# Optimization experiments

Hardware: AMD Instinct MI355X
Metric: run time of the kernel (lower is better)

The kernel has to match this reference:

```python
import jax, jax.numpy as jnp
import numpy as np

HOPS = 3  # max_hops; C has HOPS+1 tables

def setup_inputs() -> dict:
    key = jax.random.key(0)
    k1, k2, k3 = jax.random.split(key, 3)
    B, M, S, V, D = 32, 512, 10, 32000, 128
    story = jax.random.randint(k1, (B, M, S), 0, V)
    hidden = jax.random.normal(k2, (B, 1, D), dtype=jnp.float32)
    # hop+1 embedding tables, initialized N(0, 0.1) like the torch module
    C = 0.1 * jax.random.normal(k3, (HOPS + 1, V, D), dtype=jnp.float32)
    return {"story": story, "hidden": hidden, "C": C}

def reference(story, hidden, C):
    # story: [B, M, S] int tokens; hidden: [B, 1, D]; C: [HOPS+1, V, D]
    u = jnp.squeeze(hidden, axis=1)  # [B, D]
    prob_logit = None
    for h in range(HOPS):
        # embedding gather + bag-sum over sentence dim -> [B, M, D]
        embed_A = jnp.take(C[h], story, axis=0).sum(axis=2)
        # dot-product attention logits against current query u
        prob_logit = jnp.einsum('bmd,bd->bm', embed_A, u)  # [B, M]
        prob = jax.nn.softmax(prob_logit, axis=1)
        # second table gather + bag-sum, then softmax-weighted combine
        embed_C = jnp.take(C[h + 1], story, axis=0).sum(axis=2)  # [B, M, D]
        o_k = jnp.einsum('bm,bmd->bd', prob, embed_C)  # [B, D]
        u = u + o_k
    return prob_logit, u
```

## Files before the change

kernel.cpp:

```cpp
#include <hip/hip_runtime.h>

#define BB 32
#define MM 512
#define SS 10
#define VV 32000
#define DD 128
#define HOPS 3
#define BM (BB * MM)
#define NCHUNK 32
#define CHM (MM / NCHUNK)
#define PSTRIDE 132


__device__ __forceinline__ void write_partial(const int b, const int c,
                                              const int w, const int lane,
                                              float nx, float ny, float den,
                                              float* __restrict__ pout,
                                              float (*sx)[64], float (*sy)[64],
                                              float* sd) {
    sx[w][lane] = nx; sy[w][lane] = ny;
    if (lane == 0) sd[w] = den;
    __syncthreads();
    if (w == 0) {
        const float ox = sx[0][lane] + sx[1][lane] + sx[2][lane] + sx[3][lane];
        const float oy = sy[0][lane] + sy[1][lane] + sy[2][lane] + sy[3][lane];
        float* prow = pout + ((size_t)b * NCHUNK + c) * PSTRIDE;
        ((float2*)prow)[lane] = make_float2(ox, oy);
        if (lane == 0) prow[DD] = sd[0] + sd[1] + sd[2] + sd[3];
    }
}

__global__ __launch_bounds__(256) void hop0_k(const int* __restrict__ story,
                                              const float* __restrict__ C0,
                                              const float* __restrict__ C1,
                                              const float* __restrict__ hidden,
                                              float* __restrict__ E1,
                                              float* __restrict__ P0) {
    const int b = blockIdx.y, c = blockIdx.x;
    const int tid = threadIdx.x;
    const int w = tid >> 6, lane = tid & 63;
    __shared__ float su[DD];
    __shared__ float sx[4][64], sy[4][64];
    __shared__ float sd[4];

    if (tid < DD) su[tid] = hidden[b * DD + tid];
    __syncthreads();
    const float2 uv = ((const float2*)su)[lane];

    float nx = 0.f, ny = 0.f, den = 0.f;
#pragma unroll
    for (int k = 0; k < CHM / 4; ++k) {
        const int m = c * CHM + k * 4 + w;
        const int bm = b * MM + m;
        int tok[SS];
        const int* st = story + (size_t)bm * SS;
#pragma unroll
        for (int s = 0; s < SS; ++s) tok[s] = st[s];

        float ex = 0.f, ey = 0.f;
#pragma unroll
        for (int s = 0; s < SS; ++s) {
            const float2 v = ((const float2*)(C0 + (size_t)tok[s] * DD))[lane];
            ex += v.x; ey += v.y;
        }
        float l = ex * uv.x + ey * uv.y;
#pragma unroll
        for (int off = 32; off; off >>= 1) l += __shfl_xor(l, off, 64);
        const float e = expf(l);

        float rx = 0.f, ry = 0.f;
#pragma unroll
        for (int s = 0; s < SS; ++s) {
            const float2 v = ((const float2*)(C1 + (size_t)tok[s] * DD))[lane];
            rx += v.x; ry += v.y;
        }
        ((float2*)(E1 + (size_t)bm * DD))[lane] = make_float2(rx, ry);
        nx += e * rx; ny += e * ry; den += e;
    }
    write_partial(b, c, w, lane, nx, ny, den, P0, sx, sy, sd);
}

__global__ __launch_bounds__(256) void hop1_k(const int* __restrict__ story,
                                              const float* __restrict__ C2,
                                              const float* __restrict__ C3,
                                              const float* __restrict__ E1,
                                              const float* __restrict__ hidden,
                                              const float* __restrict__ P0,
                                              float* __restrict__ u1,
                                              float* __restrict__ E2,
                                              float* __restrict__ E3,
                                              float* __restrict__ P1) {
    const int b = blockIdx.y, c = blockIdx.x;
    const int tid = threadIdx.x;
    const int w = tid >> 6, lane = tid & 63;
    __shared__ float su[DD];
    __shared__ float sx[4][64], sy[4][64];
    __shared__ float sd[4];

    if (tid < DD) {
        float num = 0.f, dsum = 0.f;
        for (int cc = 0; cc < NCHUNK; ++cc) {
            const float* p = P0 + ((size_t)b * NCHUNK + cc) * PSTRIDE;
            num += p[tid];
            dsum += p[DD];
        }
        const float v = hidden[b * DD + tid] + num / dsum;
        if (c == 0) u1[b * DD + tid] = v;
        su[tid] = v;
    }
    __syncthreads();
    const float2 uv = ((const float2*)su)[lane];

    float nx = 0.f, ny = 0.f, den = 0.f;
#pragma unroll
    for (int k = 0; k < CHM / 4; ++k) {
        const int m = c * CHM + k * 4 + w;
        const int bm = b * MM + m;
        int tok[SS];
        const int* st = story + (size_t)bm * SS;
#pragma unroll
        for (int s = 0; s < SS; ++s) tok[s] = st[s];

        const float2 ev = ((const float2*)(E1 + (size_t)bm * DD))[lane];
        float l = ev.x * uv.x + ev.y * uv.y;
#pragma unroll
        for (int off = 32; off; off >>= 1) l += __shfl_xor(l, off, 64);
        const float e = expf(l);

        float r2x = 0.f, r2y = 0.f;
#pragma unroll
        for (int s = 0; s < SS; ++s) {
            const float2 v = ((const float2*)(C2 + (size_t)tok[s] * DD))[lane];
            r2x += v.x; r2y += v.y;
        }
        float r3x = 0.f, r3y = 0.f;
#pragma unroll
        for (int s = 0; s < SS; ++s) {
            const float2 v = ((const float2*)(C3 + (size_t)tok[s] * DD))[lane];
            r3x += v.x; r3y += v.y;
        }
        ((float2*)(E2 + (size_t)bm * DD))[lane] = make_float2(r2x, r2y);
        ((float2*)(E3 + (size_t)bm * DD))[lane] = make_float2(r3x, r3y);
        nx += e * r2x; ny += e * r2y; den += e;
    }
    write_partial(b, c, w, lane, nx, ny, den, P1, sx, sy, sd);
}

__global__ __launch_bounds__(1024) void hop2_final(const float* __restrict__ E2,
                                                   const float* __restrict__ E3,
                                                   const float* __restrict__ u1,
                                                   const float* __restrict__ P1,
                                                   float* __restrict__ logit,
                                                   float* __restrict__ uout) {
    const int b = blockIdx.x;
    const int tid = threadIdx.x;
    const int w = tid >> 6, lane = tid & 63;
    __shared__ float su[DD];
    __shared__ float sx[16][64], sy[16][64];
    __shared__ float sd[16];

    if (tid < DD) {
        float num = 0.f, dsum = 0.f;
        for (int cc = 0; cc < NCHUNK; ++cc) {
            const float* p = P1 + ((size_t)b * NCHUNK + cc) * PSTRIDE;
            num += p[tid];
            dsum += p[DD];
        }
        su[tid] = u1[b * DD + tid] + num / dsum;
    }
    __syncthreads();
    const float2 uv = ((const float2*)su)[lane];

    float nx = 0.f, ny = 0.f, den = 0.f;
#pragma unroll 4
    for (int m = w * 32; m < w * 32 + 32; ++m) {
        const int bm = b * MM + m;
        const float2 ev = ((const float2*)(E2 + (size_t)bm * DD))[lane];
        float l = ev.x * uv.x + ev.y * uv.y;
#pragma unroll
        for (int off = 32; off; off >>= 1) l += __shfl_xor(l, off, 64);
        if (lane == 0) logit[bm] = l;
        const float e = expf(l);
        const float2 rv = ((const float2*)(E3 + (size_t)bm * DD))[lane];
        nx += e * rv.x; ny += e * rv.y; den += e;
    }

    sx[w][lane] = nx; sy[w][lane] = ny;
    if (lane == 0) sd[w] = den;
    __syncthreads();
    if (w == 0) {
        float ox = 0.f, oy = 0.f, od = 0.f;
#pragma unroll
        for (int i = 0; i < 16; ++i) { ox += sx[i][lane]; oy += sy[i][lane]; od += sd[i]; }
        const float2 u2 = ((const float2*)su)[lane];
        ((float2*)(uout + b * DD))[lane] = make_float2(u2.x + ox / od, u2.y + oy / od);
    }
}

__global__ __launch_bounds__(256) void init_u(const float* __restrict__ hidden,
                                              float* __restrict__ u) {
    int i = blockIdx.x * 256 + threadIdx.x;
    if (i < BB * DD) u[i] = hidden[i];
}

__global__ __launch_bounds__(256) void logit_kernel(const int* __restrict__ story,
                                                    const float* __restrict__ Ch,
                                                    const float* __restrict__ u,
                                                    float* __restrict__ logit) {
    int wid = (blockIdx.x * 256 + threadIdx.x) >> 6;
    int lane = threadIdx.x & 63;
    if (wid >= BB * MM) return;
    int b = wid >> 9;
    const int* st = story + (size_t)wid * SS;
    int tok[SS];
#pragma unroll
    for (int s = 0; s < SS; ++s) tok[s] = st[s];
    float ax = 0.f, ay = 0.f;
#pragma unroll
    for (int s = 0; s < SS; ++s) {
        const float2 v = ((const float2*)(Ch + (size_t)tok[s] * DD))[lane];
        ax += v.x; ay += v.y;
    }
    const float2 uv = ((const float2*)(u + b * DD))[lane];
    float p = ax * uv.x + ay * uv.y;
#pragma unroll
    for (int off = 32; off; off >>= 1) p += __shfl_down(p, off, 64);
    if (lane == 0) logit[wid] = p;
}

__global__ __launch_bounds__(256) void softmax_kernel(const float* __restrict__ logit,
                                                      float* __restrict__ prob) {
    int b = blockIdx.x;
    int t = threadIdx.x;
    __shared__ float red[8];
    float l0 = logit[b * MM + t];
    float l1 = logit[b * MM + 256 + t];
    float mx = fmaxf(l0, l1);
#pragma unroll
    for (int off = 32; off; off >>= 1) mx = fmaxf(mx, __shfl_xor(mx, off, 64));
    if ((t & 63) == 0) red[t >> 6] = mx;
    __syncthreads();
    mx = fmaxf(fmaxf(red[0], red[1]), fmaxf(red[2], red[3]));
    float e0 = expf(l0 - mx), e1 = expf(l1 - mx);
    float s = e0 + e1;
#pragma unroll
    for (int off = 32; off; off >>= 1) s += __shfl_xor(s, off, 64);
    if ((t & 63) == 0) red[4 + (t >> 6)] = s;
    __syncthreads();
    s = red[4] + red[5] + red[6] + red[7];
    float inv = 1.0f / s;
    prob[b * MM + t] = e0 * inv;
    prob[b * MM + 256 + t] = e1 * inv;
}

__global__ __launch_bounds__(256) void partial_kernel(const int* __restrict__ story,
                                                      const float* __restrict__ Ch1,
                                                      const float* __restrict__ prob,
                                                      float* __restrict__ partial,
                                                      int chunk) {
    int b = blockIdx.y, c = blockIdx.x;
    int w = threadIdx.x >> 6, lane = threadIdx.x & 63;
    int m0 = c * chunk;
    float ax = 0.f, ay = 0.f;
    for (int m = m0 + w; m < m0 + chunk; m += 4) {
        float pw = prob[b * MM + m];
        const int* st = story + (size_t)(b * MM + m) * SS;
        int tok[SS];
#pragma unroll
        for (int s = 0; s < SS; ++s) tok[s] = st[s];
        float sx = 0.f, sy = 0.f;
#pragma unroll
        for (int s = 0; s < SS; ++s) {
            const float2 v = ((const float2*)(Ch1 + (size_t)tok[s] * DD))[lane];
            sx += v.x; sy += v.y;
        }
        ax += pw * sx; ay += pw * sy;
    }
    __shared__ float redx[4][64];
    __shared__ float redy[4][64];
    redx[w][lane] = ax;
    redy[w][lane] = ay;
    __syncthreads();
    if (w == 0) {
        float ox = redx[0][lane] + redx[1][lane] + redx[2][lane] + redx[3][lane];
        float oy = redy[0][lane] + redy[1][lane] + redy[2][lane] + redy[3][lane];
        float2* dst = (float2*)(partial + ((size_t)b * gridDim.x + c) * DD);
        dst[lane] = make_float2(ox, oy);
    }
}

__global__ __launch_bounds__(256) void update_kernel(const float* __restrict__ partial,
                                                     float* __restrict__ u, int NC) {
    int i = blockIdx.x * 256 + threadIdx.x;
    if (i >= BB * DD) return;
    int b = i >> 7, d = i & 127;
    float s = 0.f;
    for (int c = 0; c < NC; ++c) s += partial[((size_t)b * NC + c) * DD + d];
    u[i] += s;
}

extern "C" void kernel_launch(void* const* d_in, const int* in_sizes, int n_in,
                              void* d_out, int out_size, void* d_ws, size_t ws_size,
                              hipStream_t stream) {
    const int*   story  = (const int*)d_in[0];
    const float* hidden = (const float*)d_in[1];
    const float* Cmat   = (const float*)d_in[2];

    float* out   = (float*)d_out;
    float* logit = out;
    float* uout  = out + BB * MM;

    const size_t szE  = (size_t)BM * DD;
    const size_t szP  = (size_t)BB * NCHUNK * PSTRIDE;
    const size_t need = (3 * szE + 2 * szP + BB * DD) * sizeof(float);

    if (ws_size >= need) {
        float* E1 = (float*)d_ws;
        float* E2 = E1 + szE;
        float* E3 = E2 + szE;
        float* P0 = E3 + szE;
        float* P1 = P0 + szP;
        float* u1 = P1 + szP;

        const float* C0 = Cmat;
        const float* C1 = Cmat + (size_t)1 * VV * DD;
        const float* C2 = Cmat + (size_t)2 * VV * DD;
        const float* C3 = Cmat + (size_t)3 * VV * DD;

        hop0_k<<<dim3(NCHUNK, BB), 256, 0, stream>>>(story, C0, C1, hidden, E1, P0);
        hop1_k<<<dim3(NCHUNK, BB), 256, 0, stream>>>(story, C2, C3, E1, hidden,
                                                     P0, u1, E2, E3, P1);
        hop2_final<<<BB, 1024, 0, stream>>>(E2, E3, u1, P1, logit, uout);
    } else {
        float* prob = (float*)d_ws;
        int NC = 32;
        while (NC > 1 && (size_t)(BB * MM + BB * NC * DD) * 4 > ws_size) NC >>= 1;
        float* partial = prob + BB * MM;
        int chunk = MM / NC;

        init_u<<<(BB * DD + 255) / 256, 256, 0, stream>>>(hidden, uout);
        for (int h = 0; h < HOPS; ++h) {
            const float* Ca = Cmat + (size_t)h * VV * DD;
            const float* Cc = Cmat + (size_t)(h + 1) * VV * DD;
            logit_kernel<<<(BB * MM) / 4, 256, 0, stream>>>(story, Ca, uout, logit);
            softmax_kernel<<<BB, 256, 0, stream>>>(logit, prob);
            partial_kernel<<<dim3(NC, BB), 256, 0, stream>>>(story, Cc, prob, partial, chunk);
            update_kernel<<<(BB * DD + 255) / 256, 256, 0, stream>>>(partial, uout, NC);
        }
    }
}
```

Before: 77.44 us.

## Convert embedding tables to bf16 and precompute hop-0 logits via vocab GEMV

After: 113.8 us. +47.0%, slower.

```diff
diff --git a/kernel.cpp b/kernel.cpp
--- a/kernel.cpp
+++ b/kernel.cpp
@@ -10,7 +10,82 @@
 #define NCHUNK 32
 #define CHM (MM / NCHUNK)
 #define PSTRIDE 132
-
+#define UT1 ((size_t)VV * DD / 8)
+#define UTP ((size_t)VV * 32)
+
+__device__ __forceinline__ unsigned bfrn(float f) {
+    unsigned u = __float_as_uint(f);
+    return (u + 0x7FFFu + ((u >> 16) & 1u)) >> 16;
+}
+__device__ __forceinline__ unsigned pk(float a, float b) { return bfrn(a) | (bfrn(b) << 16); }
+__device__ __forceinline__ float bflo(unsigned q) { return __uint_as_float(q << 16); }
+__device__ __forceinline__ float bfhi(unsigned q) { return __uint_as_float(q & 0xFFFF0000u); }
+
+__device__ __forceinline__ void cvt_unit(const float* __restrict__ C,
+                                         unsigned* __restrict__ Cb, size_t g) {
+    const float4 f0 = ((const float4*)C)[g * 2];
+    const float4 f1 = ((const float4*)C)[g * 2 + 1];
+    uint4 o;
+    o.x = pk(f0.x, f0.y);
+    o.y = pk(f0.z, f0.w);
+    o.z = pk(f1.x, f1.y);
+    o.w = pk(f1.z, f1.w);
+    ((uint4*)Cb)[g] = o;
+}
+
+__device__ __forceinline__ void cvt_pair_unit(const float* __restrict__ CA,
+                                              const float* __restrict__ CB,
+                                              unsigned* __restrict__ dst, size_t g) {
+    const size_t v = g >> 5, j = g & 31;
+    const float4 a = ((const float4*)CA)[v * 32 + j];
+    const float4 b = ((const float4*)CB)[v * 32 + j];
+    uint4 o;
+    o.x = pk(a.x, a.y);
+    o.y = pk(b.x, b.y);
+    o.z = pk(a.z, a.w);
+    o.w = pk(b.z, b.w);
+    ((uint4*)dst)[v * 32 + j] = o;
+}
+
+
+__global__ __launch_bounds__(256) void gemv0_k(const float* __restrict__ C0,
+                                               const float* __restrict__ hidden,
+                                               float* __restrict__ cu0,
+                                               const float* __restrict__ Cmat,
+                                               unsigned* __restrict__ Cb1) {
+    const int tid = threadIdx.x;
+    const int w = tid >> 6, lane = tid & 63;
+    const int gw = blockIdx.x * 4 + w;
+    const int b = lane >> 1, half = lane & 1;
+
+    float4 ur[16];
+    const float4* h4 = (const float4*)hidden;
+#pragma unroll
+    for (int i = 0; i < 16; ++i) ur[i] = h4[b * 32 + half * 16 + i];
+
+#pragma unroll
+    for (int r = 0; r < 16; ++r) {
+        const int v = gw * 16 + r;
+        if (v < VV) {
+            const float4* Crow = (const float4*)(C0 + (size_t)v * DD) + half * 16;
+            float p = 0.f;
+#pragma unroll
+            for (int i = 0; i < 16; ++i) {
+                const float4 c = Crow[i];
+                p += c.x * ur[i].x + c.y * ur[i].y + c.z * ur[i].z + c.w * ur[i].w;
+            }
+            p += __shfl_xor(p, 1, 64);
+            if (half == 0) cu0[(size_t)v * BB + b] = p;
+        }
+    }
+
+    const size_t t0 = ((size_t)blockIdx.x * 256 + tid) * 4;
+#pragma unroll
+    for (int i = 0; i < 4; ++i) {
+        const size_t g = t0 + i;
+        if (g < UT1) cvt_unit(Cmat + (size_t)VV * DD, Cb1, g);
+    }
+}
 
 __device__ __forceinline__ void write_partial(const int b, const int c,
                                               const int w, const int lane,
@@ -31,21 +106,17 @@
 }
 
 __global__ __launch_bounds__(256) void hop0_k(const int* __restrict__ story,
-                                              const float* __restrict__ C0,
-                                              const float* __restrict__ C1,
-                                              const float* __restrict__ hidden,
-                                              float* __restrict__ E1,
-                                              float* __restrict__ P0) {
+                                              const float* __restrict__ cu0,
+                                              const unsigned* __restrict__ Cb1,
+                                              unsigned* __restrict__ E1,
+                                              float* __restrict__ P0,
+                                              const float* __restrict__ Cmat,
+                                              unsigned* __restrict__ Cb23) {
     const int b = blockIdx.y, c = blockIdx.x;
     const int tid = threadIdx.x;
     const int w = tid >> 6, lane = tid & 63;
-    __shared__ float su[DD];
     __shared__ float sx[4][64], sy[4][64];
     __shared__ float sd[4];
-
-    if (tid < DD) su[tid] = hidden[b * DD + tid];
-    __syncthreads();
-    const float2 uv = ((const float2*)su)[lane];
 
     float nx = 0.f, ny = 0.f, den = 0.f;
 #pragma unroll
@@ -57,38 +128,39 @@
 #pragma unroll
         for (int s = 0; s < SS; ++s) tok[s] = st[s];
 
-        float ex = 0.f, ey = 0.f;
+        float l = 0.f;
+#pragma unroll
+        for (int s = 0; s < SS; ++s) l += cu0[(size_t)tok[s] * BB + b];
+        const float e = expf(l);
+
+        float rx = 0.f, ry = 0.f;
 #pragma unroll
         for (int s = 0; s < SS; ++s) {
-            const float2 v = ((const float2*)(C0 + (size_t)tok[s] * DD))[lane];
-            ex += v.x; ey += v.y;
-        }
-        float l = ex * uv.x + ey * uv.y;
-#pragma unroll
-        for (int off = 32; off; off >>= 1) l += __shfl_xor(l, off, 64);
-        const float e = expf(l);
-
-        float rx = 0.f, ry = 0.f;
-#pragma unroll
-        for (int s = 0; s < SS; ++s) {
-            const float2 v = ((const float2*)(C1 + (size_t)tok[s] * DD))[lane];
-            rx += v.x; ry += v.y;
-        }
-        ((float2*)(E1 + (size_t)bm * DD))[lane] = make_float2(rx, ry);
+            const unsigned q = Cb1[(size_t)tok[s] * 64 + lane];
+            rx += bflo(q); ry += bfhi(q);
+        }
+        E1[(size_t)bm * 64 + lane] = pk(rx, ry);
         nx += e * rx; ny += e * ry; den += e;
     }
     write_partial(b, c, w, lane, nx, ny, den, P0, sx, sy, sd);
+
+    const size_t t0 = (((size_t)blockIdx.y * gridDim.x + blockIdx.x) * 256 + tid) * 4;
+#pragma unroll
+    for (int i = 0; i < 4; ++i) {
+        const size_t g = t0 + i;
+        if (g < UTP)
+            cvt_pair_unit(Cmat + (size_t)2 * VV * DD, Cmat + (size_t)3 * VV * DD,
+                          Cb23, g);
+    }
 }
 
 __global__ __launch_bounds__(256) void hop1_k(const int* __restrict__ story,
-                                              const float* __restrict__ C2,
-                                              const float* __restrict__ C3,
-                                              const float* __restrict__ E1,
+                                              const unsigned* __restrict__ Cb23,
+                                              const unsigned* __restrict__ E1,
                                               const float* __restrict__ hidden,
                                               const float* __restrict__ P0,
                                               float* __restrict__ u1,
-                                              float* __restrict__ E2,
-                                              float* __restrict__ E3,
+                                              unsigned* __restrict__ E23,
                                               float* __restrict__ P1) {
     const int b = blockIdx.y, c = blockIdx.x;
     const int tid = threadIdx.x;
@@ -121,33 +193,26 @@
 #pragma unroll
         for (int s = 0; s < SS; ++s) tok[s] = st[s];
 
-        const float2 ev = ((const float2*)(E1 + (size_t)bm * DD))[lane];
-        float l = ev.x * uv.x + ev.y * uv.y;
+        const unsigned eq = E1[(size_t)bm * 64 + lane];
+        float l = bflo(eq) * uv.x + bfhi(eq) * uv.y;
 #pragma unroll
         for (int off = 32; off; off >>= 1) l += __shfl_xor(l, off, 64);
         const float e = expf(l);
 
-        float r2x = 0.f, r2y = 0.f;
+        float r2x = 0.f, r2y = 0.f, r3x = 0.f, r3y = 0.f;
 #pragma unroll
         for (int s = 0; s < SS; ++s) {
-            const float2 v = ((const float2*)(C2 + (size_t)tok[s] * DD))[lane];
-            r2x += v.x; r2y += v.y;
-        }
-        float r3x = 0.f, r3y = 0.f;
-#pragma unroll
-        for (int s = 0; s < SS; ++s) {
-            const float2 v = ((const float2*)(C3 + (size_t)tok[s] * DD))[lane];
-            r3x += v.x; r3y += v.y;
-        }
-        ((float2*)(E2 + (size_t)bm * DD))[lane] = make_float2(r2x, r2y);
-        ((float2*)(E3 + (size_t)bm * DD))[lane] = make_float2(r3x, r3y);
+            const uint2 q = ((const uint2*)Cb23)[(size_t)tok[s] * 64 + lane];
+            r2x += bflo(q.x); r2y += bfhi(q.x);
+            r3x += bflo(q.y); r3y += bfhi(q.y);
+        }
+        ((uint2*)E23)[(size_t)bm * 64 + lane] = make_uint2(pk(r2x, r2y), pk(r3x, r3y));
         nx += e * r2x; ny += e * r2y; den += e;
     }
     write_partial(b, c, w, lane, nx, ny, den, P1, sx, sy, sd);
 }
 
-__global__ __launch_bounds__(1024) void hop2_final(const float* __restrict__ E2,
-                                                   const float* __restrict__ E3,
+__global__ __launch_bounds__(1024) void hop2_final(const unsigned* __restrict__ E23,
                                                    const float* __restrict__ u1,
                                                    const float* __restrict__ P1,
                                                    float* __restrict__ logit,
@@ -175,14 +240,13 @@
 #pragma unroll 4
     for (int m = w * 32; m < w * 32 + 32; ++m) {
         const int bm = b * MM + m;
-        const float2 ev = ((const float2*)(E2 + (size_t)bm * DD))[lane];
-        float l = ev.x * uv.x + ev.y * uv.y;
+        const uint2 q = ((const uint2*)E23)[(size_t)bm * 64 + lane];
+        float l = bflo(q.x) * uv.x + bfhi(q.x) * uv.y;
 #pragma unroll
         for (int off = 32; off; off >>= 1) l += __shfl_xor(l, off, 64);
         if (lane == 0) logit[bm] = l;
         const float e = expf(l);
-        const float2 rv = ((const float2*)(E3 + (size_t)bm * DD))[lane];
-        nx += e * rv.x; ny += e * rv.y; den += e;
+        nx += e * bflo(q.y); ny += e * bfhi(q.y); den += e;
     }
 
     sx[w][lane] = nx; sy[w][lane] = ny;
@@ -310,27 +374,31 @@
     float* logit = out;
     float* uout  = out + BB * MM;
 
-    const size_t szE  = (size_t)BM * DD;
-    const size_t szP  = (size_t)BB * NCHUNK * PSTRIDE;
-    const size_t need = (3 * szE + 2 * szP + BB * DD) * sizeof(float);
+    const size_t szCU  = (size_t)VV * BB;
+    const size_t szCb1 = (size_t)VV * 64;
+    const size_t szCbp = (size_t)VV * 128;
+    const size_t szE1  = (size_t)BM * 64;
+    const size_t szE23 = (size_t)BM * 128;
+    const size_t szP   = (size_t)BB * NCHUNK * PSTRIDE;
+    const size_t need  = (szCU + szCb1 + szCbp + szE1 + szE23 + 2 * szP + BB * DD)
+                         * sizeof(float);
 
     if (ws_size >= need) {
-        float* E1 = (float*)d_ws;
-        float* E2 = E1 + szE;
-        float* E3 = E2 + szE;
-        float* P0 = E3 + szE;
-        float* P1 = P0 + szP;
-        float* u1 = P1 + szP;
-
-        const float* C0 = Cmat;
-        const float* C1 = Cmat + (size_t)1 * VV * DD;
-        const float* C2 = Cmat + (size_t)2 * VV * DD;
-        const float* C3 = Cmat + (size_t)3 * VV * DD;
-
-        hop0_k<<<dim3(NCHUNK, BB), 256, 0, stream>>>(story, C0, C1, hidden, E1, P0);
-        hop1_k<<<dim3(NCHUNK, BB), 256, 0, stream>>>(story, C2, C3, E1, hidden,
-                                                     P0, u1, E2, E3, P1);
-        hop2_final<<<BB, 1024, 0, stream>>>(E2, E3, u1, P1, logit, uout);
+        float*    cu0  = (float*)d_ws;
+        unsigned* Cb1  = (unsigned*)d_ws + szCU;
+        unsigned* Cb23 = Cb1 + szCb1;
+        unsigned* E1   = Cb23 + szCbp;
+        unsigned* E23  = E1 + szE1;
+        float*    P0   = (float*)(E23 + szE23);
+        float*    P1   = P0 + szP;
+        float*    u1   = P1 + szP;
+
+        gemv0_k<<<512, 256, 0, stream>>>(Cmat, hidden, cu0, Cmat, Cb1);
+        hop0_k<<<dim3(NCHUNK, BB), 256, 0, stream>>>(story, cu0, Cb1, E1, P0,
+                                                     Cmat, Cb23);
+        hop1_k<<<dim3(NCHUNK, BB), 256, 0, stream>>>(story, Cb23, E1, hidden,
+                                                     P0, u1, E23, P1);
+        hop2_final<<<BB, 1024, 0, stream>>>(E23, u1, P1, logit, uout);
     } else {
         float* prob = (float*)d_ws;
         int NC = 32;
```
